# Optimization experiments

Measured on AMD Instinct MI355X. Metric: run time of the kernel, lower is better.

Reference implementation:

```python
import jax, jax.numpy as jnp
import numpy as np

N_NODES = 100000
N_EDGES = 1600000
IN_CH = 64
HID = 64
OUT_CH = 32


def _init_lin(key, fan_in, fan_out):
    # uniform(-1/sqrt(fan_in), 1/sqrt(fan_in)) like torch Linear
    b = 1.0 / np.sqrt(fan_in)
    return jax.random.uniform(key, (fan_in, fan_out), jnp.float32, -b, b)


def setup_inputs() -> dict:
    key = jax.random.key(0)
    ks = jax.random.split(key, 16)
    x = jax.random.normal(ks[0], (N_NODES, IN_CH), jnp.float32)
    edge_index = jax.random.randint(ks[1], (2, N_EDGES), 0, N_NODES, jnp.int64)
    params = {}
    dims = [(IN_CH, HID), (HID, HID), (HID, HID)]
    for i, (fi, fo) in enumerate(dims, start=1):
        params[f"Wl{i}"] = _init_lin(ks[3 * i], fi, fo)       # applied to aggregated neighbors
        params[f"Wr{i}"] = _init_lin(ks[3 * i + 1], fi, fo)   # applied to root features
        params[f"b{i}"] = jnp.zeros((fo,), jnp.float32)
    params["Wlin"] = _init_lin(ks[12], HID, OUT_CH)
    params["blin"] = jnp.zeros((OUT_CH,), jnp.float32)
    return {"x": x, "edge_index": edge_index, **params}


def _mean_aggregate(x, src, dst, n_nodes):
    # mean of source-node features over incoming edges per destination node
    msg_sum = jax.ops.segment_sum(x[src], dst, num_segments=n_nodes)
    deg = jax.ops.segment_sum(jnp.ones((src.shape[0], 1), x.dtype), dst, num_segments=n_nodes)
    return msg_sum / jnp.maximum(deg, 1.0)


def _sage_conv(x, src, dst, Wl, Wr, b):
    # PyG SAGEConv (mean aggr): out = lin_l(mean_j x_j) + lin_r(x_i)
    agg = _mean_aggregate(x, src, dst, x.shape[0])
    return agg @ Wl + b + x @ Wr


def reference(x, edge_index, Wl1, Wr1, b1, Wl2, Wr2, b2, Wl3, Wr3, b3, Wlin, blin):
    src, dst = edge_index[0], edge_index[1]
    h = jax.nn.relu(_sage_conv(x, src, dst, Wl1, Wr1, b1))
    h = jax.nn.relu(_sage_conv(h, src, dst, Wl2, Wr2, b2))
    h = jax.nn.relu(_sage_conv(h, src, dst, Wl3, Wr3, b3))
    return h @ Wlin + blin
```

## Files before the change

kernel.cpp:

```cpp
#include <hip/hip_runtime.h>
#include <hip/hip_bf16.h>

#define N_NODES 100000
#define N_EDGES 1600000
#define HID 64
#define OUT_CH 32

#define NB 196
#define P 1024
#define EPP ((N_EDGES + P - 1) / P)
#define BKCAP 10240
#define MP 72

typedef unsigned short ushort_t;
typedef short bf16x8 __attribute__((ext_vector_type(8)));
typedef float f32x4 __attribute__((ext_vector_type(4)));

__device__ __forceinline__ ushort_t f2b(float f) {
    union { float f; unsigned u; } un; un.f = f;
    unsigned r = un.u + 0x7FFF + ((un.u >> 16) & 1);
    return (ushort_t)(r >> 16);
}
__device__ __forceinline__ float b2f(ushort_t u) {
    union { unsigned u; float f; } un; un.u = ((unsigned)u) << 16;
    return un.f;
}
__device__ __forceinline__ float blo(unsigned u) {
    union { unsigned u; float f; } un; un.u = u << 16; return un.f;
}
__device__ __forceinline__ float bhi(unsigned u) {
    union { unsigned u; float f; } un; un.u = u & 0xFFFF0000u; return un.f;
}

__device__ __forceinline__ int get_dst(const int* __restrict__ ei, int is64, int e) {
    return is64 ? ((const int2*)ei)[N_EDGES + e].x : ei[N_EDGES + e];
}
__device__ __forceinline__ int get_src(const int* __restrict__ ei, int is64, int e) {
    return is64 ? ((const int2*)ei)[e].x : ei[e];
}

__device__ __forceinline__ void detect_is64(const int* __restrict__ ei,
                                            int* __restrict__ sflag, int tid) {
    if (tid < 64) {
        int v = ei[2 * tid + 1];
        unsigned long long ball = __ballot(v == 0);
        if (tid == 0) *sflag = (ball == ~0ull) ? 1 : 0;
    }
}

#define CONV_BLOCKS ((N_NODES * HID / 4) / 256)
__global__ void __launch_bounds__(256) convhist_kernel(
        const float* __restrict__ x, ushort_t* __restrict__ xb,
        const int* __restrict__ ei, int* __restrict__ histG,
        const float* __restrict__ W0, const float* __restrict__ W1,
        const float* __restrict__ W2, const float* __restrict__ W3,
        const float* __restrict__ W4, const float* __restrict__ W5,
        ushort_t* __restrict__ wpk) {
    int bid = blockIdx.x;
    if (bid >= CONV_BLOCKS) {
        const float* Ws[6] = {W0, W1, W2, W3, W4, W5};
        int w = bid - CONV_BLOCKS;
        const float* W = Ws[w];
        ushort_t* d = wpk + w * 4096;
        for (int idx = threadIdx.x; idx < 4096; idx += 256) {
            int j = idx & 7;
            int ln = (idx >> 3) & 63;
            int t = idx >> 9;
            int ks = t & 1, nt = t >> 1;
            int k = ks * 32 + (ln >> 4) * 8 + j;
            int n = nt * 16 + (ln & 15);
            d[idx] = f2b(W[k * HID + n]);
        }
        return;
    }
    int i = bid * 256 + threadIdx.x;
    if (i < N_NODES * HID / 4) {
        float4 v = ((const float4*)x)[i];
        ushort4 o;
        o.x = f2b(v.x); o.y = f2b(v.y); o.z = f2b(v.z); o.w = f2b(v.w);
        ((ushort4*)xb)[i] = o;
    }
    if (bid >= P) return;
    __shared__ int sflag;
    __shared__ int lh[NB];
    int tid = threadIdx.x;
    detect_is64(ei, &sflag, tid);
    for (int k = tid; k < NB; k += 256) lh[k] = 0;
    __syncthreads();
    int is64 = sflag;
    int e0 = bid * EPP;
    int e1 = min(e0 + EPP, N_EDGES);
    for (int e = e0 + tid; e < e1; e += 256) {
        int d = get_dst(ei, is64, e);
        atomicAdd(&lh[d >> 9], 1);
    }
    __syncthreads();
    for (int k = tid; k < NB; k += 256) histG[k * P + bid] = lh[k];
}

__global__ void __launch_bounds__(256) scan_kernel(int* __restrict__ histG,
                                                   int* __restrict__ btot) {
    __shared__ int ps[256];
    int b = blockIdx.x;
    int tid = threadIdx.x;
    int base4 = b * P + 4 * tid;
    int v0 = histG[base4], v1 = histG[base4 + 1], v2 = histG[base4 + 2], v3 = histG[base4 + 3];
    int pv = v0 + v1 + v2 + v3;
    ps[tid] = pv;
    __syncthreads();
    for (int d = 1; d < 256; d <<= 1) {
        int t = (tid >= d) ? ps[tid - d] : 0;
        __syncthreads();
        ps[tid] += t;
        __syncthreads();
    }
    int e = ps[tid] - pv;
    histG[base4] = e; e += v0;
    histG[base4 + 1] = e; e += v1;
    histG[base4 + 2] = e; e += v2;
    histG[base4 + 3] = e;
    if (tid == 255) btot[b] = ps[255];
}

__global__ void __launch_bounds__(256) place_kernel(
        const int* __restrict__ ei, const int* __restrict__ histG,
        const int* __restrict__ btot, int* __restrict__ bkt) {
    __shared__ int lcur[NB];
    __shared__ int ss[256];
    __shared__ int sflag;
    int tid = threadIdx.x;
    detect_is64(ei, &sflag, tid);
    int v = (tid < NB) ? btot[tid] : 0;
    ss[tid] = v;
    __syncthreads();
    for (int d = 1; d < 256; d <<= 1) {
        int t = (tid >= d) ? ss[tid - d] : 0;
        __syncthreads();
        ss[tid] += t;
        __syncthreads();
    }
    if (tid < NB) lcur[tid] = (ss[tid] - v) + histG[tid * P + blockIdx.x];
    __syncthreads();
    int is64 = sflag;
    int e0 = blockIdx.x * EPP;
    int e1 = min(e0 + EPP, N_EDGES);
    for (int e = e0 + tid; e < e1; e += 256) {
        int s = get_src(ei, is64, e);
        int d = get_dst(ei, is64, e);
        int val = ((d & 511) << 17) | s;
        int p = atomicAdd(&lcur[d >> 9], 1);
        bkt[p] = val;
    }
}

__global__ void __launch_bounds__(256) bucket_fill_kernel(
        const int* __restrict__ btot, const int* __restrict__ bkt,
        int* __restrict__ csr, unsigned int* __restrict__ offpk) {
    __shared__ int lcnt[512];
    __shared__ int loff[512];
    __shared__ int lcur[512];
    __shared__ int ps[256];
    __shared__ int scsr[BKCAP];
    __shared__ int sbase;
    int b = blockIdx.x;
    int tid = threadIdx.x;
    int m = btot[b];
    int vb = (tid < NB) ? btot[tid] : 0;
    ps[tid] = vb;
    __syncthreads();
    for (int d = 1; d < 256; d <<= 1) {
        int t = (tid >= d) ? ps[tid - d] : 0;
        __syncthreads();
        ps[tid] += t;
        __syncthreads();
    }
    if (tid == b) sbase = ps[tid] - vb;
    __syncthreads();
    int base = sbase;
    int n0 = b << 9;
    int nn = min(512, N_NODES - n0);

    lcnt[tid] = 0;
    lcnt[tid + 256] = 0;
    __syncthreads();
    for (int i = tid; i < m; i += 256) atomicAdd(&lcnt[bkt[base + i] >> 17], 1);
    __syncthreads();
    int a0 = lcnt[2 * tid], a1 = lcnt[2 * tid + 1];
    int pv = a0 + a1;
    ps[tid] = pv;
    __syncthreads();
    for (int d = 1; d < 256; d <<= 1) {
        int t = (tid >= d) ? ps[tid - d] : 0;
        __syncthreads();
        ps[tid] += t;
        __syncthreads();
    }
    int excl = ps[tid] - pv;
    loff[2 * tid] = excl;
    loff[2 * tid + 1] = excl + a0;
    lcur[2 * tid] = excl;
    lcur[2 * tid + 1] = excl + a0;
    __syncthreads();
    bool fit = (m <= BKCAP);
    for (int i = tid; i < m; i += 256) {
        int val = bkt[base + i];
        int dl = val >> 17;
        int p = atomicAdd(&lcur[dl], 1);
        if (fit) scsr[p] = val & 0x1FFFF;
        else csr[base + p] = val & 0x1FFFF;
    }
    __syncthreads();
    if (fit)
        for (int i = tid; i < m; i += 256) csr[base + i] = scsr[i];
    for (int i = tid; i < nn; i += 256)
        offpk[n0 + i] = (unsigned int)((base + loff[i]) | (lcnt[i] << 21));
}

__global__ void __launch_bounds__(256) gather_kernel(
        const ushort_t* __restrict__ hb, const unsigned int* __restrict__ offpk,
        const int* __restrict__ csr, ushort_t* __restrict__ aggb) {
    int tid = threadIdx.x;
    int wv = tid >> 6, ln = tid & 63;
    int g = ln >> 3;
    int l = ln & 7;
    int node = blockIdx.x * 32 + wv * 8 + g;
    unsigned int v = offpk[node];
    int off = (int)(v & 0x1FFFFFu);
    int cnt = (int)(v >> 21);
    float a0 = 0.f, a1 = 0.f, a2 = 0.f, a3 = 0.f;
    float a4 = 0.f, a5 = 0.f, a6 = 0.f, a7 = 0.f;
    int gbase = g << 3;
    for (int b = 0; b < cnt; b += 16) {
        int rem = cnt - b;
        int e0 = (l < rem) ? csr[off + b + l] : 0;
        int e1 = (l + 8 < rem) ? csr[off + b + 8 + l] : 0;
        int4 u[16];
#pragma unroll
        for (int j = 0; j < 8; ++j)
            u[j] = ((const int4*)(hb + (size_t)__shfl(e0, gbase + j) * HID))[l];
#pragma unroll
        for (int j = 0; j < 8; ++j)
            u[8 + j] = ((const int4*)(hb + (size_t)__shfl(e1, gbase + j) * HID))[l];
#pragma unroll
        for (int j = 0; j < 16; ++j) {
            if (j >= rem) { u[j].x = 0; u[j].y = 0; u[j].z = 0; u[j].w = 0; }
            a0 += blo(u[j].x); a1 += bhi(u[j].x);
            a2 += blo(u[j].y); a3 += bhi(u[j].y);
            a4 += blo(u[j].z); a5 += bhi(u[j].z);
            a6 += blo(u[j].w); a7 += bhi(u[j].w);
        }
    }
    float inv = 1.f / fmaxf((float)cnt, 1.f);
    int4 w;
    w.x = (int)((unsigned)f2b(a0 * inv) | ((unsigned)f2b(a1 * inv) << 16));
    w.y = (int)((unsigned)f2b(a2 * inv) | ((unsigned)f2b(a3 * inv) << 16));
    w.z = (int)((unsigned)f2b(a4 * inv) | ((unsigned)f2b(a5 * inv) << 16));
    w.w = (int)((unsigned)f2b(a6 * inv) | ((unsigned)f2b(a7 * inv) << 16));
    *(int4*)(aggb + (size_t)node * HID + l * 8) = w;
}

template <bool FUSE_HEAD>
__global__ void __launch_bounds__(256) layer_mfma(
        const ushort_t* __restrict__ aggb, const ushort_t* __restrict__ rootb,
        const ushort_t* __restrict__ wpk, const float* __restrict__ bias,
        ushort_t* __restrict__ outb,
        const float* __restrict__ Wlin, const float* __restrict__ blin,
        float* __restrict__ out) {
    __shared__ __align__(16) ushort_t sWlF[4096];
    __shared__ __align__(16) ushort_t sWrF[4096];
    __shared__ __align__(16) ushort_t sA[64 * MP];
    __shared__ __align__(16) ushort_t sH[64 * MP];
    __shared__ float sbias[HID];
    __shared__ float sWo[FUSE_HEAD ? HID * OUT_CH : 1];
    __shared__ float sbo[FUSE_HEAD ? OUT_CH : 1];
    int tid = threadIdx.x;
    {
        const int4* w4 = (const int4*)wpk;
        int4* sl4 = (int4*)sWlF;
        int4* sr4 = (int4*)sWrF;
#pragma unroll
        for (int p = 0; p < 2; ++p) {
            int i = tid + 256 * p;
            sl4[i] = w4[i];
            sr4[i] = w4[512 + i];
        }
    }
    if (tid < HID) sbias[tid] = bias[tid];
    size_t tbase = (size_t)blockIdx.x * 64 * HID;
    {
        const int4* ga = (const int4*)(aggb + tbase);
        const int4* gh = (const int4*)(rootb + tbase);
#pragma unroll
        for (int p = 0; p < 2; ++p) {
            int q = tid + 256 * p;
            int r = q >> 3, u = q & 7;
            *(int4*)(sA + r * MP + u * 8) = ga[q];
            *(int4*)(sH + r * MP + u * 8) = gh[q];
        }
    }
    __syncthreads();

    int wave = tid >> 6, lane = tid & 63;
    int quad = lane >> 4, col = lane & 15;
    int arow = wave * 16 + col;
    bf16x8 aA0 = *(const bf16x8*)(sA + arow * MP + quad * 8);
    bf16x8 aA1 = *(const bf16x8*)(sA + arow * MP + 32 + quad * 8);
    bf16x8 aH0 = *(const bf16x8*)(sH + arow * MP + quad * 8);
    bf16x8 aH1 = *(const bf16x8*)(sH + arow * MP + 32 + quad * 8);
    int node0 = blockIdx.x * 64;
    ushort_t hv[4][4];
#pragma unroll
    for (int nt = 0; nt < 4; ++nt) {
        f32x4 acc = {0.f, 0.f, 0.f, 0.f};
        const bf16x8* bl = (const bf16x8*)(sWlF + nt * 1024);
        const bf16x8* br = (const bf16x8*)(sWrF + nt * 1024);
        acc = __builtin_amdgcn_mfma_f32_16x16x32_bf16(aA0, bl[lane], acc, 0, 0, 0);
        acc = __builtin_amdgcn_mfma_f32_16x16x32_bf16(aA1, bl[64 + lane], acc, 0, 0, 0);
        acc = __builtin_amdgcn_mfma_f32_16x16x32_bf16(aH0, br[lane], acc, 0, 0, 0);
        acc = __builtin_amdgcn_mfma_f32_16x16x32_bf16(aH1, br[64 + lane], acc, 0, 0, 0);
        float bv = sbias[nt * 16 + col];
#pragma unroll
        for (int r = 0; r < 4; ++r) {
            ushort_t hb16 = f2b(fmaxf(acc[r] + bv, 0.f));
            if constexpr (FUSE_HEAD) {
                hv[nt][r] = hb16;
            } else {
                int n = node0 + wave * 16 + quad * 4 + r;
                if (n < N_NODES)
                    outb[(size_t)n * HID + nt * 16 + col] = hb16;
            }
        }
    }

    if constexpr (FUSE_HEAD) {
        __syncthreads();
#pragma unroll
        for (int nt = 0; nt < 4; ++nt)
#pragma unroll
            for (int r = 0; r < 4; ++r)
                sA[(wave * 16 + quad * 4 + r) * MP + nt * 16 + col] = hv[nt][r];
        {
            const int4* W4 = (const int4*)Wlin;
            int4* sW4 = (int4*)sWo;
#pragma unroll
            for (int p = 0; p < 2; ++p) sW4[tid + 256 * p] = W4[tid + 256 * p];
            if (tid < OUT_CH) sbo[tid] = blin[tid];
        }
        __syncthreads();

        int c0 = (tid & 7) << 2;
        int n0 = (tid >> 3) << 1;
        float acc2[2][4];
#pragma unroll
        for (int i = 0; i < 2; ++i)
#pragma unroll
            for (int j = 0; j < 4; ++j) acc2[i][j] = sbo[c0 + j];

#pragma unroll 4
        for (int kk = 0; kk < 32; ++kk) {
            float4 w0 = *(const float4*)&sWo[(2 * kk) * OUT_CH + c0];
            float4 w1 = *(const float4*)&sWo[(2 * kk + 1) * OUT_CH + c0];
            const float* w0p = (const float*)&w0;
            const float* w1p = (const float*)&w1;
#pragma unroll
            for (int i = 0; i < 2; ++i) {
                unsigned uh = *(const unsigned*)(sA + (n0 + i) * MP + 2 * kk);
                float h0 = blo(uh), h1 = bhi(uh);
#pragma unroll
                for (int j = 0; j < 4; ++j) acc2[i][j] += h0 * w0p[j] + h1 * w1p[j];
            }
        }

#pragma unroll
        for (int i = 0; i < 2; ++i) {
            int n = node0 + n0 + i;
            if (n < N_NODES) {
                float4 o4;
                o4.x = acc2[i][0]; o4.y = acc2[i][1];
                o4.z = acc2[i][2]; o4.w = acc2[i][3];
                *(float4*)(out + (size_t)n * OUT_CH + c0) = o4;
            }
        }
    }
}

extern "C" void kernel_launch(void* const* d_in, const int* in_sizes, int n_in,
                              void* d_out, int out_size, void* d_ws, size_t ws_size,
                              hipStream_t stream) {
    const float* x    = (const float*)d_in[0];
    const int*   ei   = (const int*)d_in[1];
    const float* Wl1  = (const float*)d_in[2];
    const float* Wr1  = (const float*)d_in[3];
    const float* b1   = (const float*)d_in[4];
    const float* Wl2  = (const float*)d_in[5];
    const float* Wr2  = (const float*)d_in[6];
    const float* b2   = (const float*)d_in[7];
    const float* Wl3  = (const float*)d_in[8];
    const float* Wr3  = (const float*)d_in[9];
    const float* b3   = (const float*)d_in[10];
    const float* Wlin = (const float*)d_in[11];
    const float* blin = (const float*)d_in[12];
    float* out = (float*)d_out;

    int* ip              = (int*)d_ws;
    unsigned int* offpk  = (unsigned int*)ip;
    int* btot            = (int*)(offpk + 100096);
    int* histG           = btot + 256;
    int* csr             = histG + NB * P;
    ushort_t* aggb       = (ushort_t*)(csr + N_EDGES);
    ushort_t* featb      = aggb + 6408192;
    ushort_t* wpk        = featb + 6408192;
    int* bkt             = (int*)aggb;

    const int GATHER_BLOCKS = N_NODES / 32;
    const int TILE_BLOCKS   = (N_NODES + 63) / 64;

    convhist_kernel<<<CONV_BLOCKS + 6, 256, 0, stream>>>(
        x, featb, ei, histG, Wl1, Wr1, Wl2, Wr2, Wl3, Wr3, wpk);
    scan_kernel<<<NB, 256, 0, stream>>>(histG, btot);
    place_kernel<<<P, 256, 0, stream>>>(ei, histG, btot, bkt);
    bucket_fill_kernel<<<NB, 256, 0, stream>>>(btot, bkt, csr, offpk);

    gather_kernel<<<GATHER_BLOCKS, 256, 0, stream>>>(featb, offpk, csr, aggb);
    layer_mfma<false><<<TILE_BLOCKS, 256, 0, stream>>>(
        aggb, featb, wpk, b1, featb, nullptr, nullptr, nullptr);

    gather_kernel<<<GATHER_BLOCKS, 256, 0, stream>>>(featb, offpk, csr, aggb);
    layer_mfma<false><<<TILE_BLOCKS, 256, 0, stream>>>(
        aggb, featb, wpk + 8192, b2, featb, nullptr, nullptr, nullptr);

    gather_kernel<<<GATHER_BLOCKS, 256, 0, stream>>>(featb, offpk, csr, aggb);
    layer_mfma<true><<<TILE_BLOCKS, 256, 0, stream>>>(
        aggb, featb, wpk + 16384, b3, nullptr, Wlin, blin, out);
}
```

Before: 260.0 us.

## Fuse CSR build kernels into one persistent kernel with grid barriers

The four preprocessing kernels (convert+histogram, scan, place, bucket fill) are merged into one kernel of 512 persistent blocks that synchronise through a global atomic grid barrier. The edge partition count drops from 1024 to 512 to match the persistent grid. The aim is to remove three kernel launch gaps and their drain/fill bubbles. The barrier depends on all 512 blocks being co-resident. The large shared-memory footprint may lower occupancy, and an added memset launch resets the barrier counter.

Measured after the change: 539.5 us. +107.5%, slower.

```diff
diff --git a/kernel.cpp b/kernel.cpp
--- a/kernel.cpp
+++ b/kernel.cpp
@@ -7,10 +7,11 @@
 #define OUT_CH 32
 
 #define NB 196
-#define P 1024
-#define EPP ((N_EDGES + P - 1) / P)
+#define P2 512
+#define EPP2 ((N_EDGES + P2 - 1) / P2)
 #define BKCAP 10240
 #define MP 72
+#define CONVT (N_NODES * HID / 4 / 256)
 
 typedef unsigned short ushort_t;
 typedef short bf16x8 __attribute__((ext_vector_type(8)));
@@ -21,10 +22,6 @@
     unsigned r = un.u + 0x7FFF + ((un.u >> 16) & 1);
     return (ushort_t)(r >> 16);
 }
-__device__ __forceinline__ float b2f(ushort_t u) {
-    union { unsigned u; float f; } un; un.u = ((unsigned)u) << 16;
-    return un.f;
-}
 __device__ __forceinline__ float blo(unsigned u) {
     union { unsigned u; float f; } un; un.u = u << 16; return un.f;
 }
@@ -39,181 +36,187 @@
     return is64 ? ((const int2*)ei)[e].x : ei[e];
 }
 
-__device__ __forceinline__ void detect_is64(const int* __restrict__ ei,
-                                            int* __restrict__ sflag, int tid) {
+__device__ __forceinline__ void gridbar(int* cnt, int* gen) {
+    __syncthreads();
+    if (threadIdx.x == 0) {
+        __threadfence();
+        int g = __hip_atomic_load(gen, __ATOMIC_ACQUIRE, __HIP_MEMORY_SCOPE_AGENT);
+        int a = __hip_atomic_fetch_add(cnt, 1, __ATOMIC_ACQ_REL,
+                                       __HIP_MEMORY_SCOPE_AGENT) + 1;
+        if (a == P2) {
+            __hip_atomic_store(cnt, 0, __ATOMIC_RELAXED, __HIP_MEMORY_SCOPE_AGENT);
+            __hip_atomic_store(gen, g + 1, __ATOMIC_RELEASE, __HIP_MEMORY_SCOPE_AGENT);
+        } else {
+            while (__hip_atomic_load(gen, __ATOMIC_ACQUIRE,
+                                     __HIP_MEMORY_SCOPE_AGENT) == g)
+                __builtin_amdgcn_s_sleep(1);
+        }
+        __threadfence();
+    }
+    __syncthreads();
+}
+
+__global__ void __launch_bounds__(256) csrbuild_kernel(
+        const float* __restrict__ x, ushort_t* __restrict__ xb,
+        const int* __restrict__ ei,
+        const float* __restrict__ W0, const float* __restrict__ W1,
+        const float* __restrict__ W2, const float* __restrict__ W3,
+        const float* __restrict__ W4, const float* __restrict__ W5,
+        ushort_t* __restrict__ wpk,
+        int* __restrict__ histG, int* __restrict__ btot,
+        int* __restrict__ bkt, int* __restrict__ csr,
+        unsigned int* __restrict__ offpk, int* __restrict__ bar) {
+    __shared__ int smem[12040];
+    __shared__ int sflag;
+    int bid = blockIdx.x, tid = threadIdx.x;
+
     if (tid < 64) {
         int v = ei[2 * tid + 1];
         unsigned long long ball = __ballot(v == 0);
-        if (tid == 0) *sflag = (ball == ~0ull) ? 1 : 0;
-    }
-}
-
-#define CONV_BLOCKS ((N_NODES * HID / 4) / 256)
-__global__ void __launch_bounds__(256) convhist_kernel(
-        const float* __restrict__ x, ushort_t* __restrict__ xb,
-        const int* __restrict__ ei, int* __restrict__ histG,
-        const float* __restrict__ W0, const float* __restrict__ W1,
-        const float* __restrict__ W2, const float* __restrict__ W3,
-        const float* __restrict__ W4, const float* __restrict__ W5,
-        ushort_t* __restrict__ wpk) {
-    int bid = blockIdx.x;
-    if (bid >= CONV_BLOCKS) {
-        const float* Ws[6] = {W0, W1, W2, W3, W4, W5};
-        int w = bid - CONV_BLOCKS;
-        const float* W = Ws[w];
-        ushort_t* d = wpk + w * 4096;
-        for (int idx = threadIdx.x; idx < 4096; idx += 256) {
-            int j = idx & 7;
-            int ln = (idx >> 3) & 63;
-            int t = idx >> 9;
-            int ks = t & 1, nt = t >> 1;
-            int k = ks * 32 + (ln >> 4) * 8 + j;
-            int n = nt * 16 + (ln & 15);
-            d[idx] = f2b(W[k * HID + n]);
-        }
-        return;
-    }
-    int i = bid * 256 + threadIdx.x;
-    if (i < N_NODES * HID / 4) {
-        float4 v = ((const float4*)x)[i];
-        ushort4 o;
-        o.x = f2b(v.x); o.y = f2b(v.y); o.z = f2b(v.z); o.w = f2b(v.w);
-        ((ushort4*)xb)[i] = o;
-    }
-    if (bid >= P) return;
-    __shared__ int sflag;
-    __shared__ int lh[NB];
-    int tid = threadIdx.x;
-    detect_is64(ei, &sflag, tid);
-    for (int k = tid; k < NB; k += 256) lh[k] = 0;
-    __syncthreads();
+        if (tid == 0) sflag = (ball == ~0ull) ? 1 : 0;
+    }
+    {
+        int* lh = smem;
+        for (int k = tid; k < NB; k += 256) lh[k] = 0;
+        __syncthreads();
+        int is64loc = sflag;
+        for (int t = bid; t < CONVT; t += P2) {
+            int i = t * 256 + tid;
+            float4 v = ((const float4*)x)[i];
+            ushort4 o;
+            o.x = f2b(v.x); o.y = f2b(v.y); o.z = f2b(v.z); o.w = f2b(v.w);
+            ((ushort4*)xb)[i] = o;
+        }
+        if (bid < 6) {
+            const float* Ws[6] = {W0, W1, W2, W3, W4, W5};
+            const float* W = Ws[bid];
+            ushort_t* d = wpk + bid * 4096;
+            for (int idx = tid; idx < 4096; idx += 256) {
+                int j = idx & 7;
+                int ln = (idx >> 3) & 63;
+                int t = idx >> 9;
+                int ks = t & 1, nt = t >> 1;
+                int k = ks * 32 + (ln >> 4) * 8 + j;
+                int n = nt * 16 + (ln & 15);
+                d[idx] = f2b(W[k * HID + n]);
+            }
+        }
+        int e0 = bid * EPP2;
+        int e1 = min(e0 + EPP2, N_EDGES);
+        for (int e = e0 + tid; e < e1; e += 256) {
+            int d = get_dst(ei, is64loc, e);
+            atomicAdd(&lh[d >> 9], 1);
+        }
+        __syncthreads();
+        for (int k = tid; k < NB; k += 256) histG[k * P2 + bid] = lh[k];
+    }
     int is64 = sflag;
-    int e0 = bid * EPP;
-    int e1 = min(e0 + EPP, N_EDGES);
-    for (int e = e0 + tid; e < e1; e += 256) {
-        int d = get_dst(ei, is64, e);
-        atomicAdd(&lh[d >> 9], 1);
-    }
-    __syncthreads();
-    for (int k = tid; k < NB; k += 256) histG[k * P + bid] = lh[k];
-}
-
-__global__ void __launch_bounds__(256) scan_kernel(int* __restrict__ histG,
-                                                   int* __restrict__ btot) {
-    __shared__ int ps[256];
-    int b = blockIdx.x;
-    int tid = threadIdx.x;
-    int base4 = b * P + 4 * tid;
-    int v0 = histG[base4], v1 = histG[base4 + 1], v2 = histG[base4 + 2], v3 = histG[base4 + 3];
-    int pv = v0 + v1 + v2 + v3;
-    ps[tid] = pv;
-    __syncthreads();
-    for (int d = 1; d < 256; d <<= 1) {
-        int t = (tid >= d) ? ps[tid - d] : 0;
-        __syncthreads();
-        ps[tid] += t;
-        __syncthreads();
-    }
-    int e = ps[tid] - pv;
-    histG[base4] = e; e += v0;
-    histG[base4 + 1] = e; e += v1;
-    histG[base4 + 2] = e; e += v2;
-    histG[base4 + 3] = e;
-    if (tid == 255) btot[b] = ps[255];
-}
-
-__global__ void __launch_bounds__(256) place_kernel(
-        const int* __restrict__ ei, const int* __restrict__ histG,
-        const int* __restrict__ btot, int* __restrict__ bkt) {
-    __shared__ int lcur[NB];
-    __shared__ int ss[256];
-    __shared__ int sflag;
-    int tid = threadIdx.x;
-    detect_is64(ei, &sflag, tid);
-    int v = (tid < NB) ? btot[tid] : 0;
-    ss[tid] = v;
-    __syncthreads();
-    for (int d = 1; d < 256; d <<= 1) {
-        int t = (tid >= d) ? ss[tid - d] : 0;
-        __syncthreads();
-        ss[tid] += t;
-        __syncthreads();
-    }
-    if (tid < NB) lcur[tid] = (ss[tid] - v) + histG[tid * P + blockIdx.x];
-    __syncthreads();
-    int is64 = sflag;
-    int e0 = blockIdx.x * EPP;
-    int e1 = min(e0 + EPP, N_EDGES);
-    for (int e = e0 + tid; e < e1; e += 256) {
-        int s = get_src(ei, is64, e);
-        int d = get_dst(ei, is64, e);
-        int val = ((d & 511) << 17) | s;
-        int p = atomicAdd(&lcur[d >> 9], 1);
-        bkt[p] = val;
-    }
-}
-
-__global__ void __launch_bounds__(256) bucket_fill_kernel(
-        const int* __restrict__ btot, const int* __restrict__ bkt,
-        int* __restrict__ csr, unsigned int* __restrict__ offpk) {
-    __shared__ int lcnt[512];
-    __shared__ int loff[512];
-    __shared__ int lcur[512];
-    __shared__ int ps[256];
-    __shared__ int scsr[BKCAP];
-    __shared__ int sbase;
-    int b = blockIdx.x;
-    int tid = threadIdx.x;
-    int m = btot[b];
-    int vb = (tid < NB) ? btot[tid] : 0;
-    ps[tid] = vb;
-    __syncthreads();
-    for (int d = 1; d < 256; d <<= 1) {
-        int t = (tid >= d) ? ps[tid - d] : 0;
-        __syncthreads();
-        ps[tid] += t;
-        __syncthreads();
-    }
-    if (tid == b) sbase = ps[tid] - vb;
-    __syncthreads();
-    int base = sbase;
-    int n0 = b << 9;
-    int nn = min(512, N_NODES - n0);
-
-    lcnt[tid] = 0;
-    lcnt[tid + 256] = 0;
-    __syncthreads();
-    for (int i = tid; i < m; i += 256) atomicAdd(&lcnt[bkt[base + i] >> 17], 1);
-    __syncthreads();
-    int a0 = lcnt[2 * tid], a1 = lcnt[2 * tid + 1];
-    int pv = a0 + a1;
-    ps[tid] = pv;
-    __syncthreads();
-    for (int d = 1; d < 256; d <<= 1) {
-        int t = (tid >= d) ? ps[tid - d] : 0;
-        __syncthreads();
-        ps[tid] += t;
-        __syncthreads();
-    }
-    int excl = ps[tid] - pv;
-    loff[2 * tid] = excl;
-    loff[2 * tid + 1] = excl + a0;
-    lcur[2 * tid] = excl;
-    lcur[2 * tid + 1] = excl + a0;
-    __syncthreads();
-    bool fit = (m <= BKCAP);
-    for (int i = tid; i < m; i += 256) {
-        int val = bkt[base + i];
-        int dl = val >> 17;
-        int p = atomicAdd(&lcur[dl], 1);
-        if (fit) scsr[p] = val & 0x1FFFF;
-        else csr[base + p] = val & 0x1FFFF;
-    }
-    __syncthreads();
-    if (fit)
-        for (int i = tid; i < m; i += 256) csr[base + i] = scsr[i];
-    for (int i = tid; i < nn; i += 256)
-        offpk[n0 + i] = (unsigned int)((base + loff[i]) | (lcnt[i] << 21));
+    gridbar(bar, bar + 1);
+
+    if (bid < NB) {
+        int* ps = smem;
+        int base2 = bid * P2 + 2 * tid;
+        int v0 = histG[base2], v1 = histG[base2 + 1];
+        int pv = v0 + v1;
+        ps[tid] = pv;
+        __syncthreads();
+        for (int d = 1; d < 256; d <<= 1) {
+            int t = (tid >= d) ? ps[tid - d] : 0;
+            __syncthreads();
+            ps[tid] += t;
+            __syncthreads();
+        }
+        int e = ps[tid] - pv;
+        histG[base2] = e;
+        histG[base2 + 1] = e + v0;
+        if (tid == 255) btot[bid] = ps[255];
+    }
+    gridbar(bar, bar + 1);
+
+    {
+        int* lcur = smem;
+        int* ss = smem + 256;
+        int v = (tid < NB) ? btot[tid] : 0;
+        ss[tid] = v;
+        __syncthreads();
+        for (int d = 1; d < 256; d <<= 1) {
+            int t = (tid >= d) ? ss[tid - d] : 0;
+            __syncthreads();
+            ss[tid] += t;
+            __syncthreads();
+        }
+        if (tid < NB) lcur[tid] = (ss[tid] - v) + histG[tid * P2 + bid];
+        __syncthreads();
+        int e0 = bid * EPP2;
+        int e1 = min(e0 + EPP2, N_EDGES);
+        for (int e = e0 + tid; e < e1; e += 256) {
+            int s = get_src(ei, is64, e);
+            int d = get_dst(ei, is64, e);
+            int val = ((d & 511) << 17) | s;
+            int p = atomicAdd(&lcur[d >> 9], 1);
+            bkt[p] = val;
+        }
+    }
+    gridbar(bar, bar + 1);
+
+    if (bid < NB) {
+        int* ps   = smem;
+        int* lcnt = smem + 256;
+        int* loff = smem + 768;
+        int* lcur = smem + 1280;
+        int* scsr = smem + 1792;
+        int* sbase = smem + 12032;
+        int m = btot[bid];
+        int vb = (tid < NB) ? btot[tid] : 0;
+        ps[tid] = vb;
+        __syncthreads();
+        for (int d = 1; d < 256; d <<= 1) {
+            int t = (tid >= d) ? ps[tid - d] : 0;
+            __syncthreads();
+            ps[tid] += t;
+            __syncthreads();
+        }
+        if (tid == bid) *sbase = ps[tid] - vb;
+        __syncthreads();
+        int base = *sbase;
+        int n0 = bid << 9;
+        int nn = min(512, N_NODES - n0);
+
+        lcnt[tid] = 0;
+        lcnt[tid + 256] = 0;
+        __syncthreads();
+        for (int i = tid; i < m; i += 256) atomicAdd(&lcnt[bkt[base + i] >> 17], 1);
+        __syncthreads();
+        int a0 = lcnt[2 * tid], a1 = lcnt[2 * tid + 1];
+        int pv = a0 + a1;
+        ps[tid] = pv;
+        __syncthreads();
+        for (int d = 1; d < 256; d <<= 1) {
+            int t = (tid >= d) ? ps[tid - d] : 0;
+            __syncthreads();
+            ps[tid] += t;
+            __syncthreads();
+        }
+        int excl = ps[tid] - pv;
+        loff[2 * tid] = excl;
+        loff[2 * tid + 1] = excl + a0;
+        lcur[2 * tid] = excl;
+        lcur[2 * tid + 1] = excl + a0;
+        __syncthreads();
+        bool fit = (m <= BKCAP);
+        for (int i = tid; i < m; i += 256) {
+            int val = bkt[base + i];
+            int dl = val >> 17;
+            int p = atomicAdd(&lcur[dl], 1);
+            if (fit) scsr[p] = val & 0x1FFFF;
+            else csr[base + p] = val & 0x1FFFF;
+        }
+        __syncthreads();
+        if (fit)
+            for (int i = tid; i < m; i += 256) csr[base + i] = scsr[i];
+        for (int i = tid; i < nn; i += 256)
+            offpk[n0 + i] = (unsigned int)((base + loff[i]) | (lcnt[i] << 21));
+    }
 }
 
 __global__ void __launch_bounds__(256) gather_kernel(
@@ -406,20 +409,20 @@
     unsigned int* offpk  = (unsigned int*)ip;
     int* btot            = (int*)(offpk + 100096);
     int* histG           = btot + 256;
-    int* csr             = histG + NB * P;
+    int* csr             = histG + 200704;
     ushort_t* aggb       = (ushort_t*)(csr + N_EDGES);
     ushort_t* featb      = aggb + 6408192;
     ushort_t* wpk        = featb + 6408192;
+    int* bar             = (int*)(wpk + 24576);
     int* bkt             = (int*)aggb;
 
     const int GATHER_BLOCKS = N_NODES / 32;
     const int TILE_BLOCKS   = (N_NODES + 63) / 64;
 
-    convhist_kernel<<<CONV_BLOCKS + 6, 256, 0, stream>>>(
-        x, featb, ei, histG, Wl1, Wr1, Wl2, Wr2, Wl3, Wr3, wpk);
-    scan_kernel<<<NB, 256, 0, stream>>>(histG, btot);
-    place_kernel<<<P, 256, 0, stream>>>(ei, histG, btot, bkt);
-    bucket_fill_kernel<<<NB, 256, 0, stream>>>(btot, bkt, csr, offpk);
+    hipMemsetAsync(bar, 0, 16, stream);
+    csrbuild_kernel<<<P2, 256, 0, stream>>>(
+        x, featb, ei, Wl1, Wr1, Wl2, Wr2, Wl3, Wr3, wpk,
+        histG, btot, bkt, csr, offpk, bar);
 
     gather_kernel<<<GATHER_BLOCKS, 256, 0, stream>>>(featb, offpk, csr, aggb);
     layer_mfma<false><<<TILE_BLOCKS, 256, 0, stream>>>(
```

## Fuse neighbor gather with per-layer MFMA transform and ping-pong feature buffers

Applied to the files above, without the earlier changes.

Merges the mean-aggregation gather kernel and the MFMA layer kernel into one 512-thread kernel per layer. The aggregated tile stays in shared memory instead of round-tripping through a global agg buffer. Because a layer now reads features it must not overwrite, output goes to a second feature buffer, with A and B alternating across layers. This removes three launches and the agg write/read traffic. In exchange, each block does more work and holds more shared memory, and the gather's latency can no longer be hidden by separate high-occupancy launches.

Measured after the change: 245.9 us, median of 2. -5.4%, faster.

```diff
diff --git a/kernel.cpp b/kernel.cpp
--- a/kernel.cpp
+++ b/kernel.cpp
@@ -20,10 +20,6 @@
     union { float f; unsigned u; } un; un.f = f;
     unsigned r = un.u + 0x7FFF + ((un.u >> 16) & 1);
     return (ushort_t)(r >> 16);
-}
-__device__ __forceinline__ float b2f(ushort_t u) {
-    union { unsigned u; float f; } un; un.u = ((unsigned)u) << 16;
-    return un.f;
 }
 __device__ __forceinline__ float blo(unsigned u) {
     union { unsigned u; float f; } un; un.u = u << 16; return un.f;
@@ -216,15 +212,43 @@
         offpk[n0 + i] = (unsigned int)((base + loff[i]) | (lcnt[i] << 21));
 }
 
-__global__ void __launch_bounds__(256) gather_kernel(
-        const ushort_t* __restrict__ hb, const unsigned int* __restrict__ offpk,
-        const int* __restrict__ csr, ushort_t* __restrict__ aggb) {
-    int tid = threadIdx.x;
+template <bool FUSE_HEAD>
+__global__ void __launch_bounds__(512, 4) fused_gather_layer(
+        const ushort_t* __restrict__ featin,
+        const unsigned int* __restrict__ offpk, const int* __restrict__ csr,
+        const ushort_t* __restrict__ wpk, const float* __restrict__ bias,
+        ushort_t* __restrict__ featout,
+        const float* __restrict__ Wlin, const float* __restrict__ blin,
+        float* __restrict__ out) {
+    __shared__ __align__(16) ushort_t sWlF[4096];
+    __shared__ __align__(16) ushort_t sWrF[4096];
+    __shared__ __align__(16) ushort_t sA[64 * MP];
+    __shared__ __align__(16) ushort_t sH[64 * MP];
+    __shared__ float sbias[HID];
+    __shared__ float sWo[FUSE_HEAD ? HID * OUT_CH : 1];
+    __shared__ float sbo[FUSE_HEAD ? OUT_CH : 1];
+    int tid = threadIdx.x;
+    int node0 = blockIdx.x * 64;
+
+    ((int4*)sWlF)[tid] = ((const int4*)wpk)[tid];
+    ((int4*)sWrF)[tid] = ((const int4*)wpk)[512 + tid];
+    if (tid < HID) sbias[tid] = bias[tid];
+    if constexpr (FUSE_HEAD) {
+        ((int4*)sWo)[tid] = ((const int4*)Wlin)[tid];
+        if (tid < OUT_CH) sbo[tid] = blin[tid];
+    }
+    {
+        const int4* gh = (const int4*)(featin + (size_t)node0 * HID);
+        int r = tid >> 3, u = tid & 7;
+        *(int4*)(sH + r * MP + u * 8) = gh[tid];
+    }
+
     int wv = tid >> 6, ln = tid & 63;
     int g = ln >> 3;
     int l = ln & 7;
-    int node = blockIdx.x * 32 + wv * 8 + g;
-    unsigned int v = offpk[node];
+    int nl = wv * 8 + g;
+    int node = node0 + nl;
+    unsigned int v = (node < N_NODES) ? offpk[node] : 0u;
     int off = (int)(v & 0x1FFFFFu);
     int cnt = (int)(v >> 21);
     float a0 = 0.f, a1 = 0.f, a2 = 0.f, a3 = 0.f;
@@ -237,10 +261,10 @@
         int4 u[16];
 #pragma unroll
         for (int j = 0; j < 8; ++j)
-            u[j] = ((const int4*)(hb + (size_t)__shfl(e0, gbase + j) * HID))[l];
+            u[j] = ((const int4*)(featin + (size_t)__shfl(e0, gbase + j) * HID))[l];
 #pragma unroll
         for (int j = 0; j < 8; ++j)
-            u[8 + j] = ((const int4*)(hb + (size_t)__shfl(e1, gbase + j) * HID))[l];
+            u[8 + j] = ((const int4*)(featin + (size_t)__shfl(e1, gbase + j) * HID))[l];
 #pragma unroll
         for (int j = 0; j < 16; ++j) {
             if (j >= rem) { u[j].x = 0; u[j].y = 0; u[j].z = 0; u[j].w = 0; }
@@ -250,67 +274,29 @@
             a6 += blo(u[j].w); a7 += bhi(u[j].w);
         }
     }
-    float inv = 1.f / fmaxf((float)cnt, 1.f);
-    int4 w;
-    w.x = (int)((unsigned)f2b(a0 * inv) | ((unsigned)f2b(a1 * inv) << 16));
-    w.y = (int)((unsigned)f2b(a2 * inv) | ((unsigned)f2b(a3 * inv) << 16));
-    w.z = (int)((unsigned)f2b(a4 * inv) | ((unsigned)f2b(a5 * inv) << 16));
-    w.w = (int)((unsigned)f2b(a6 * inv) | ((unsigned)f2b(a7 * inv) << 16));
-    *(int4*)(aggb + (size_t)node * HID + l * 8) = w;
-}
-
-template <bool FUSE_HEAD>
-__global__ void __launch_bounds__(256) layer_mfma(
-        const ushort_t* __restrict__ aggb, const ushort_t* __restrict__ rootb,
-        const ushort_t* __restrict__ wpk, const float* __restrict__ bias,
-        ushort_t* __restrict__ outb,
-        const float* __restrict__ Wlin, const float* __restrict__ blin,
-        float* __restrict__ out) {
-    __shared__ __align__(16) ushort_t sWlF[4096];
-    __shared__ __align__(16) ushort_t sWrF[4096];
-    __shared__ __align__(16) ushort_t sA[64 * MP];
-    __shared__ __align__(16) ushort_t sH[64 * MP];
-    __shared__ float sbias[HID];
-    __shared__ float sWo[FUSE_HEAD ? HID * OUT_CH : 1];
-    __shared__ float sbo[FUSE_HEAD ? OUT_CH : 1];
-    int tid = threadIdx.x;
     {
-        const int4* w4 = (const int4*)wpk;
-        int4* sl4 = (int4*)sWlF;
-        int4* sr4 = (int4*)sWrF;
-#pragma unroll
-        for (int p = 0; p < 2; ++p) {
-            int i = tid + 256 * p;
-            sl4[i] = w4[i];
-            sr4[i] = w4[512 + i];
-        }
-    }
-    if (tid < HID) sbias[tid] = bias[tid];
-    size_t tbase = (size_t)blockIdx.x * 64 * HID;
-    {
-        const int4* ga = (const int4*)(aggb + tbase);
-        const int4* gh = (const int4*)(rootb + tbase);
-#pragma unroll
-        for (int p = 0; p < 2; ++p) {
-            int q = tid + 256 * p;
-            int r = q >> 3, u = q & 7;
-            *(int4*)(sA + r * MP + u * 8) = ga[q];
-            *(int4*)(sH + r * MP + u * 8) = gh[q];
-        }
-    }
-    __syncthreads();
-
-    int wave = tid >> 6, lane = tid & 63;
+        float inv = 1.f / fmaxf((float)cnt, 1.f);
+        int4 w;
+        w.x = (int)((unsigned)f2b(a0 * inv) | ((unsigned)f2b(a1 * inv) << 16));
+        w.y = (int)((unsigned)f2b(a2 * inv) | ((unsigned)f2b(a3 * inv) << 16));
+        w.z = (int)((unsigned)f2b(a4 * inv) | ((unsigned)f2b(a5 * inv) << 16));
+        w.w = (int)((unsigned)f2b(a6 * inv) | ((unsigned)f2b(a7 * inv) << 16));
+        *(int4*)(sA + nl * MP + l * 8) = w;
+    }
+    __syncthreads();
+
+    int lane = ln;
     int quad = lane >> 4, col = lane & 15;
-    int arow = wave * 16 + col;
+    int mt = wv >> 1, npb = (wv & 1) * 2;
+    int arow = mt * 16 + col;
     bf16x8 aA0 = *(const bf16x8*)(sA + arow * MP + quad * 8);
     bf16x8 aA1 = *(const bf16x8*)(sA + arow * MP + 32 + quad * 8);
     bf16x8 aH0 = *(const bf16x8*)(sH + arow * MP + quad * 8);
     bf16x8 aH1 = *(const bf16x8*)(sH + arow * MP + 32 + quad * 8);
-    int node0 = blockIdx.x * 64;
-    ushort_t hv[4][4];
-#pragma unroll
-    for (int nt = 0; nt < 4; ++nt) {
+    ushort_t hv[2][4];
+#pragma unroll
+    for (int t = 0; t < 2; ++t) {
+        int nt = npb + t;
         f32x4 acc = {0.f, 0.f, 0.f, 0.f};
         const bf16x8* bl = (const bf16x8*)(sWlF + nt * 1024);
         const bf16x8* br = (const bf16x8*)(sWrF + nt * 1024);
@@ -323,11 +309,11 @@
         for (int r = 0; r < 4; ++r) {
             ushort_t hb16 = f2b(fmaxf(acc[r] + bv, 0.f));
             if constexpr (FUSE_HEAD) {
-                hv[nt][r] = hb16;
+                hv[t][r] = hb16;
             } else {
-                int n = node0 + wave * 16 + quad * 4 + r;
+                int n = node0 + mt * 16 + quad * 4 + r;
                 if (n < N_NODES)
-                    outb[(size_t)n * HID + nt * 16 + col] = hb16;
+                    featout[(size_t)n * HID + nt * 16 + col] = hb16;
             }
         }
     }
@@ -335,51 +321,33 @@
     if constexpr (FUSE_HEAD) {
         __syncthreads();
 #pragma unroll
-        for (int nt = 0; nt < 4; ++nt)
+        for (int t = 0; t < 2; ++t)
 #pragma unroll
             for (int r = 0; r < 4; ++r)
-                sA[(wave * 16 + quad * 4 + r) * MP + nt * 16 + col] = hv[nt][r];
-        {
-            const int4* W4 = (const int4*)Wlin;
-            int4* sW4 = (int4*)sWo;
-#pragma unroll
-            for (int p = 0; p < 2; ++p) sW4[tid + 256 * p] = W4[tid + 256 * p];
-            if (tid < OUT_CH) sbo[tid] = blin[tid];
-        }
+                sA[(mt * 16 + quad * 4 + r) * MP + (npb + t) * 16 + col] = hv[t][r];
         __syncthreads();
 
         int c0 = (tid & 7) << 2;
-        int n0 = (tid >> 3) << 1;
-        float acc2[2][4];
-#pragma unroll
-        for (int i = 0; i < 2; ++i)
-#pragma unroll
-            for (int j = 0; j < 4; ++j) acc2[i][j] = sbo[c0 + j];
-
+        int n0 = tid >> 3;
+        float acc2[4];
+#pragma unroll
+        for (int j = 0; j < 4; ++j) acc2[j] = sbo[c0 + j];
 #pragma unroll 4
         for (int kk = 0; kk < 32; ++kk) {
             float4 w0 = *(const float4*)&sWo[(2 * kk) * OUT_CH + c0];
             float4 w1 = *(const float4*)&sWo[(2 * kk + 1) * OUT_CH + c0];
             const float* w0p = (const float*)&w0;
             const float* w1p = (const float*)&w1;
-#pragma unroll
-            for (int i = 0; i < 2; ++i) {
-                unsigned uh = *(const unsigned*)(sA + (n0 + i) * MP + 2 * kk);
-                float h0 = blo(uh), h1 = bhi(uh);
-#pragma unroll
-                for (int j = 0; j < 4; ++j) acc2[i][j] += h0 * w0p[j] + h1 * w1p[j];
-            }
-        }
-
-#pragma unroll
-        for (int i = 0; i < 2; ++i) {
-            int n = node0 + n0 + i;
-            if (n < N_NODES) {
-                float4 o4;
-                o4.x = acc2[i][0]; o4.y = acc2[i][1];
-                o4.z = acc2[i][2]; o4.w = acc2[i][3];
-                *(float4*)(out + (size_t)n * OUT_CH + c0) = o4;
-            }
+            unsigned uh = *(const unsigned*)(sA + n0 * MP + 2 * kk);
+            float h0 = blo(uh), h1 = bhi(uh);
+#pragma unroll
+            for (int j = 0; j < 4; ++j) acc2[j] += h0 * w0p[j] + h1 * w1p[j];
+        }
+        int n = node0 + n0;
+        if (n < N_NODES) {
+            float4 o4;
+            o4.x = acc2[0]; o4.y = acc2[1]; o4.z = acc2[2]; o4.w = acc2[3];
+            *(float4*)(out + (size_t)n * OUT_CH + c0) = o4;
         }
     }
 }
@@ -407,29 +375,25 @@
     int* btot            = (int*)(offpk + 100096);
     int* histG           = btot + 256;
     int* csr             = histG + NB * P;
-    ushort_t* aggb       = (ushort_t*)(csr + N_EDGES);
-    ushort_t* featb      = aggb + 6408192;
-    ushort_t* wpk        = featb + 6408192;
-    int* bkt             = (int*)aggb;
-
-    const int GATHER_BLOCKS = N_NODES / 32;
-    const int TILE_BLOCKS   = (N_NODES + 63) / 64;
+    int* bkt             = csr + N_EDGES;
+    ushort_t* featbA     = (ushort_t*)(bkt + N_EDGES);
+    ushort_t* featbB     = featbA + 6408192;
+    ushort_t* wpk        = featbB + 6408192;
+
+    const int TILE_BLOCKS = (N_NODES + 63) / 64;
 
     convhist_kernel<<<CONV_BLOCKS + 6, 256, 0, stream>>>(
-        x, featb, ei, histG, Wl1, Wr1, Wl2, Wr2, Wl3, Wr3, wpk);
+        x, featbA, ei, histG, Wl1, Wr1, Wl2, Wr2, Wl3, Wr3, wpk);
     scan_kernel<<<NB, 256, 0, stream>>>(histG, btot);
     place_kernel<<<P, 256, 0, stream>>>(ei, histG, btot, bkt);
     bucket_fill_kernel<<<NB, 256, 0, stream>>>(btot, bkt, csr, offpk);
 
-    gather_kernel<<<GATHER_BLOCKS, 256, 0, stream>>>(featb, offpk, csr, aggb);
-    layer_mfma<false><<<TILE_BLOCKS, 256, 0, stream>>>(
-        aggb, featb, wpk, b1, featb, nullptr, nullptr, nullptr);
-
-    gather_kernel<<<GATHER_BLOCKS, 256, 0, stream>>>(featb, offpk, csr, aggb);
-    layer_mfma<false><<<TILE_BLOCKS, 256, 0, stream>>>(
-        aggb, featb, wpk + 8192, b2, featb, nullptr, nullptr, nullptr);
-
-    gather_kernel<<<GATHER_BLOCKS, 256, 0, stream>>>(featb, offpk, csr, aggb);
-    layer_mfma<true><<<TILE_BLOCKS, 256, 0, stream>>>(
-        aggb, featb, wpk + 16384, b3, nullptr, Wlin, blin, out);
-}
+    fused_gather_layer<false><<<TILE_BLOCKS, 512, 0, stream>>>(
+        featbA, offpk, csr, wpk, b1, featbB, nullptr, nullptr, nullptr);
+
+    fused_gather_layer<false><<<TILE_BLOCKS, 512, 0, stream>>>(
+        featbB, offpk, csr, wpk + 8192, b2, featbA, nullptr, nullptr, nullptr);
+
+    fused_gather_layer<true><<<TILE_BLOCKS, 512, 0, stream>>>(
+        featbA, offpk, csr, wpk + 16384, b3, nullptr, Wlin, blin, out);
+}
```
